# Performance work log

Measured on AMD Instinct MI355X. Metric: run time of the kernel, lower is better.

The kernel has to match this reference:

```python
import jax, jax.numpy as jnp
import numpy as np

N = 10000      # nodes
S = 4          # num_samples (walks per node)
L = 8          # walk length
F_IN = 128     # in_features == out_features (required by SelfSupervise fc)
H = 128        # out_features (GRU hidden)
ORIG = 64      # original_features
SUB = 100      # self-supervision subsample


def _gru(x, h0, Wih, Whh, bih, bhh):
    """Single-layer unidirectional GRU. x: (L, *batch, F); h0: (*batch, H)."""
    def step(hprev, xt):
        gi = xt @ Wih.T + bih            # (*batch, 3H)
        gh = hprev @ Whh.T + bhh
        ir, iz, inn = jnp.split(gi, 3, axis=-1)
        hr, hz, hn = jnp.split(gh, 3, axis=-1)
        r = jax.nn.sigmoid(ir + hr)
        z = jax.nn.sigmoid(iz + hz)
        n = jnp.tanh(inn + r * hn)
        hnew = (1.0 - z) * n + z * hprev
        return hnew, hnew
    hT, ys = jax.lax.scan(step, h0, x)
    return ys, hT                         # ys: (L, *batch, H), hT: (*batch, H)


def setup_inputs() -> dict:
    key = jax.random.key(0)
    ks = jax.random.split(key, 14)
    s = 0.1  # weight scale for numerical sanity
    return {
        "h":     jax.random.normal(ks[0], (N, F_IN), jnp.float32),
        "y0":    jax.random.uniform(ks[1], (N, ORIG), jnp.float32),  # binary-ish targets in [0,1]
        "Wih_w": s * jax.random.normal(ks[2], (3 * H, L), jnp.float32),
        "Whh_w": s * jax.random.normal(ks[3], (3 * H, H), jnp.float32),
        "bih_w": s * jax.random.normal(ks[4], (3 * H,), jnp.float32),
        "bhh_w": s * jax.random.normal(ks[5], (3 * H,), jnp.float32),
        "Wih":   s * jax.random.normal(ks[6], (3 * H, F_IN + H), jnp.float32),
        "Whh":   s * jax.random.normal(ks[7], (3 * H, H), jnp.float32),
        "bih":   s * jax.random.normal(ks[8], (3 * H,), jnp.float32),
        "bhh":   s * jax.random.normal(ks[9], (3 * H,), jnp.float32),
        "W_ss":  s * jax.random.normal(ks[10], (ORIG, F_IN), jnp.float32),
        "b_ss":  s * jax.random.normal(ks[11], (ORIG,), jnp.float32),
        "walks": jax.random.randint(ks[12], (S, N, L), 0, N),
        "idxs":  jax.random.randint(ks[13], (SUB,), 0, N),
    }


def reference(h, y0, Wih_w, Whh_w, bih_w, bhh_w, Wih, Whh, bih, bhh, W_ss, b_ss, walks, idxs):
    # uniqueness: index of first occurrence of each node within its walk, in [0, L)
    uniq = jnp.argmax(walks[..., :, None] == walks[..., None, :], axis=-1)  # (S, N, L)
    walks_f = jnp.flip(walks, axis=-1)
    uniq_f = jnp.flip(uniq, axis=-1)
    u1h = jax.nn.one_hot(uniq_f, L, dtype=h.dtype)          # (S, N, L, L)

    hw = jnp.take(h, walks_f, axis=0)                       # (S, N, L, F_IN) gather

    h0 = jnp.zeros((S, N, H), dtype=h.dtype)
    x_walk = jnp.moveaxis(u1h, -2, 0)                       # (L, S, N, L)
    y_walk, h_walk = _gru(x_walk, h0, Wih_w, Whh_w, bih_w, bhh_w)  # (L,S,N,H), (S,N,H)
    # torch: h_walk.mean(0, keepdim=True) over layer dim of size 1 -> identity

    x_main = jnp.concatenate([jnp.moveaxis(hw, -2, 0), y_walk], axis=-1)  # (L, S, N, F_IN+H)
    y_seq, hT = _gru(x_main, h_walk, Wih, Whh, bih, bhh)    # (L,S,N,H), (S,N,H)
    y = jnp.moveaxis(y_seq, 0, -2)                          # (S, N, L, H)

    # self-supervision: subsample nodes, next-step BCE
    y_t = jnp.take(y0, walks_f, axis=0)[:, idxs, 1:, :]     # (S, SUB, L-1, ORIG)
    y_hat = y[:, idxs, :-1, :] @ W_ss.T + b_ss              # (S, SUB, L-1, ORIG)
    pos_w = 1.0 / jnp.mean(y_t)
    loss = jnp.mean(pos_w * y_t * jax.nn.softplus(-y_hat)
                    + (1.0 - y_t) * jax.nn.softplus(y_hat))

    # torch: h.mean(0) over layer dim of size 1 -> hT; activation = Identity; dropout = eval
    return hT, loss
```

## Files before the change

kernel.cpp:

```cpp
#include <hip/hip_runtime.h>
#include <math.h>

#define NN    10000
#define SSS   4
#define LL    8
#define HH    128
#define NSEQ  40000
#define SUBN  100
#define ORIGF 64
#define MA    32
#define TA    512

typedef unsigned short u16;
typedef short bf16x8 __attribute__((ext_vector_type(8)));
typedef float f32x4 __attribute__((ext_vector_type(4)));

#define L2E 1.4426950408889634f

#define WL_OFF    0
#define BWRZ_OFF  6144
#define BWIN_OFF  7168
#define BWHN_OFF  7680
#define BMRZ_OFF  8192
#define BMIN_OFF  9216
#define BMHN_OFF  9728
#define HB_OFF    10240
#define HBBUF     2176
#define HB_STR    136
#define HB_SSTR   (2*HBBUF)
#define XB_OFF    27648
#define XB_STR    136
#define XB_SSTR   (128*136)
#define SCR_OFF   97280
#define SSH_STR   132
#define SWF_OFF   114176
#define SUF_OFF   115200
#define SCNT_OFF  116224
#define SANY_OFF  116352
#define LDS_TOTAL 116384

#define WB_BYTE_OFF 64
#define W_HHW_N 49152
#define W_HH_N  49152
#define W_IH_N  98304
#define W_TOTAL (W_HHW_N + W_HH_N + W_IH_N)
#define WS_NEED ((size_t)WB_BYTE_OFF + (size_t)W_TOTAL * 2 + (size_t)NN * HH * 2)

__device__ __forceinline__ float bf2f(u16 u) {
  return __uint_as_float(((unsigned)u) << 16);
}
__device__ __forceinline__ u16 f2bf(float f) {
  unsigned u = __float_as_uint(f);
  u += 0x7fffu + ((u >> 16) & 1u);
  return (u16)(u >> 16);
}
__device__ __forceinline__ bf16x8 pack8(float4 v0, float4 v1) {
  bf16x8 r;
  r[0] = (short)f2bf(v0.x); r[1] = (short)f2bf(v0.y);
  r[2] = (short)f2bf(v0.z); r[3] = (short)f2bf(v0.w);
  r[4] = (short)f2bf(v1.x); r[5] = (short)f2bf(v1.y);
  r[6] = (short)f2bf(v1.z); r[7] = (short)f2bf(v1.w);
  return r;
}
__device__ __forceinline__ float sig2_(float xs) {
  return __builtin_amdgcn_rcpf(1.f + __builtin_amdgcn_exp2f(-xs));
}
__device__ __forceinline__ float tanh2_(float xs) {
  return 1.f - 2.f * __builtin_amdgcn_rcpf(__builtin_amdgcn_exp2f(xs) + 1.f);
}
__device__ __forceinline__ float softplusf_(float x) {
  return fmaxf(x, 0.f) + log1pf(__expf(-fabsf(x)));
}

__global__ void k_zero(float* ws) {
  if (threadIdx.x < 4) ws[threadIdx.x] = 0.f;
}

__global__ void k_prep(const float* __restrict__ whhw, const float* __restrict__ whh,
                       const float* __restrict__ wih, float* __restrict__ ws) {
  const int i = blockIdx.x * 256 + threadIdx.x;
  u16* wb = (u16*)((char*)ws + WB_BYTE_OFF);
  if (i < W_HHW_N) {
    const int row = i >> 7;
    wb[i] = f2bf(whhw[i] * ((row < 256) ? L2E : 2.f * L2E));
  } else if (i < W_HHW_N + W_HH_N) {
    const int j = i - W_HHW_N, row = j >> 7;
    wb[i] = f2bf(whh[j] * ((row < 256) ? L2E : 2.f * L2E));
  } else {
    const int j = i - W_HHW_N - W_HH_N, row = j >> 8;
    wb[i] = f2bf(wih[j] * ((row < 256) ? L2E : 2.f * L2E));
  }
}

__global__ void k_prep_h(const float* __restrict__ h, float* __restrict__ ws) {
  const int i = blockIdx.x * 256 + threadIdx.x;
  u16* hb16 = (u16*)((char*)ws + WB_BYTE_OFF) + W_TOTAL;
  hb16[i] = f2bf(h[i]);
}

template<bool BF>
__global__ __launch_bounds__(TA, 2) void k_rum(
    const float* __restrict__ hfeat, const float* __restrict__ y0,
    const float* __restrict__ WihW,  const float* __restrict__ bihW,
    const float* __restrict__ bhhW,
    const float* __restrict__ bih,   const float* __restrict__ bhh,
    const float* __restrict__ W_ss,  const float* __restrict__ b_ss,
    const int* __restrict__ walks,   const int* __restrict__ idxs,
    float* __restrict__ out, float* __restrict__ ws)
{
  extern __shared__ char sm[];
  u16*   WLb  = (u16*)(sm + WL_OFF);
  float* bwrz = (float*)(sm + BWRZ_OFF);
  float* bwin = (float*)(sm + BWIN_OFF);
  float* bwhn = (float*)(sm + BWHN_OFF);
  float* bmrz = (float*)(sm + BMRZ_OFF);
  float* bmin = (float*)(sm + BMIN_OFF);
  float* bmhn = (float*)(sm + BMHN_OFF);
  u16*   hb   = (u16*)(sm + HB_OFF);
  u16*   xb   = (u16*)(sm + XB_OFF);
  float* scr  = (float*)(sm + SCR_OFF);
  int*   swf  = (int*)(sm + SWF_OFF);
  int*   suf  = (int*)(sm + SUF_OFF);
  int*   scnt = (int*)(sm + SCNT_OFF);
  int*   sany = (int*)(sm + SANY_OFF);

  const u16* wb     = (const u16*)((const char*)ws + WB_BYTE_OFF);
  const u16* whhw_b = wb;
  const u16* whh_b  = wb + W_HHW_N;
  const u16* wih_b  = wb + W_HHW_N + W_HH_N;
  const u16* hf16   = wb + W_TOTAL;

  const int tid = threadIdx.x;
  const int lane = tid & 63, c = lane & 15, qd = lane >> 4;
  const int wv = tid >> 6;
  const int i0 = wv * 16 + c;
  const int q0 = blockIdx.x * MA;

  if (tid < MA) {
    const int m = tid;
    scnt[m] = 0;
    const int q = q0 + m;
    int w[LL];
    #pragma unroll
    for (int l = 0; l < LL; ++l) w[l] = walks[q * LL + l];
    #pragma unroll
    for (int l = 0; l < LL; ++l) {
      int u = l;
      #pragma unroll
      for (int l2 = LL - 1; l2 >= 0; --l2) if (w[l2] == w[l]) u = l2;
      swf[m * LL + (LL - 1 - l)] = w[l];
      suf[m * LL + (LL - 1 - l)] = u;
    }
  }
  if (tid == 0) *sany = 0;
  for (int idx = tid; idx < 3072; idx += TA)
    WLb[idx] = f2bf(WihW[idx] * ((idx < 2048) ? L2E : 2.f * L2E));
  if (tid < 256) {
    bwrz[tid] = (bihW[tid] + bhhW[tid]) * L2E;
    bmrz[tid] = (bih[tid] + bhh[tid]) * L2E;
  }
  if (tid < 128) {
    bwin[tid] = 2.f * L2E * bihW[256 + tid]; bwhn[tid] = 2.f * L2E * bhhW[256 + tid];
    bmin[tid] = 2.f * L2E * bih[256 + tid];  bmhn[tid] = 2.f * L2E * bhh[256 + tid];
  }
  __syncthreads();

  for (int p = tid; p < MA * SUBN; p += TA) {
    const int m = p / SUBN, i = p % SUBN;
    if (idxs[i] == (q0 + m) % NN) { atomicAdd(&scnt[m], 1); *sany = 1; }
  }

  const float bw1 = bwrz[i0], bw2 = bwrz[HH + i0], bw3 = bwin[i0], bw4 = bwhn[i0];
  const float bm1 = bmrz[i0], bm2 = bmrz[HH + i0], bm3 = bmin[i0], bm4 = bmhn[i0];

  float hreg[2][4] = {{0.f, 0.f, 0.f, 0.f}, {0.f, 0.f, 0.f, 0.f}};

  {
    bf16x8 BA[3][4];
    #pragma unroll
    for (int tl = 0; tl < 3; ++tl) {
      const int row = (tl * 8 + wv) * 16 + c;
      #pragma unroll
      for (int k = 0; k < 4; ++k)
        BA[tl][k] = *(const bf16x8*)(whhw_b + row * HH + k * 32 + qd * 8);
    }
    #pragma unroll 2
    for (int t = 0; t < LL; ++t) {
      f32x4 D[2][3];
      #pragma unroll
      for (int s = 0; s < 2; ++s) {
        #pragma unroll
        for (int tl = 0; tl < 3; ++tl) D[s][tl] = (f32x4){0.f, 0.f, 0.f, 0.f};
        if (t > 0) {
          const u16* hbc = hb + s * HB_SSTR + (t & 1) * HBBUF;
          bf16x8 a[4];
          #pragma unroll
          for (int k = 0; k < 4; ++k)
            a[k] = *(const bf16x8*)(hbc + c * HB_STR + k * 32 + qd * 8);
          #pragma unroll
          for (int tl = 0; tl < 3; ++tl) {
            f32x4 d = D[s][tl];
            #pragma unroll
            for (int k = 0; k < 4; ++k)
              d = __builtin_amdgcn_mfma_f32_16x16x32_bf16(a[k], BA[tl][k], d, 0, 0, 0);
            D[s][tl] = d;
          }
        }
      }
      #pragma unroll
      for (int s = 0; s < 2; ++s) {
        u16* hbn = hb + s * HB_SSTR + ((t + 1) & 1) * HBBUF;
        u16* xbs = xb + s * XB_SSTR;
        #pragma unroll
        for (int reg = 0; reg < 4; ++reg) {
          const int ml = qd * 4 + reg;
          const int u = suf[(s * 16 + ml) * LL + t];
          const float r = sig2_(bf2f(WLb[i0 * LL + u]) + D[s][0][reg] + bw1);
          const float z = sig2_(bf2f(WLb[(HH + i0) * LL + u]) + D[s][1][reg] + bw2);
          const float n = tanh2_(bf2f(WLb[(2 * HH + i0) * LL + u]) + bw3
                                 + r * (D[s][2][reg] + bw4));
          const float hn = n + z * (hreg[s][reg] - n);
          hreg[s][reg] = hn;
          const u16 hv = f2bf(hn);
          hbn[ml * HB_STR + i0] = hv;
          xbs[(t * 16 + ml) * XB_STR + i0] = hv;
        }
      }
      __syncthreads();
    }
  }

  const bool anyf = (*sany != 0);

  bf16x8 BW[3][8], BC[3][4];
  #pragma unroll
  for (int tl = 0; tl < 3; ++tl) {
    const int row = (tl * 8 + wv) * 16 + c;
    #pragma unroll
    for (int kk = 0; kk < 8; ++kk)
      BW[tl][kk] = *(const bf16x8*)(wih_b + row * 256 + kk * 32 + qd * 8);
    #pragma unroll
    for (int k = 0; k < 4; ++k)
      BC[tl][k] = *(const bf16x8*)(whh_b + row * HH + k * 32 + qd * 8);
  }

  float pAcc = 0.f, pBcc = 0.f, pScc = 0.f;

  #pragma unroll 2
  for (int t = 0; t < LL; ++t) {
    f32x4 Drz[2][2];
    f32x4 Dnr[2];
    f32x4 Dni[2];
    #pragma unroll
    for (int s = 0; s < 2; ++s) {
      const int node = swf[(s * 16 + c) * LL + t];
      bf16x8 ah[4];
      if constexpr (BF) {
        const u16* hp = hf16 + (size_t)node * HH + qd * 8;
        #pragma unroll
        for (int k = 0; k < 4; ++k) ah[k] = *(const bf16x8*)(hp + k * 32);
      } else {
        const float* hp = hfeat + (size_t)node * HH + qd * 8;
        #pragma unroll
        for (int k = 0; k < 4; ++k)
          ah[k] = pack8(*(const float4*)(hp + k * 32),
                        *(const float4*)(hp + k * 32 + 4));
      }
      const u16* xbs = xb + s * XB_SSTR;
      bf16x8 ay[4];
      #pragma unroll
      for (int k = 0; k < 4; ++k)
        ay[k] = *(const bf16x8*)(xbs + (t * 16 + c) * XB_STR + k * 32 + qd * 8);
      const u16* hbc = hb + s * HB_SSTR + (t & 1) * HBBUF;
      bf16x8 a[4];
      #pragma unroll
      for (int k = 0; k < 4; ++k)
        a[k] = *(const bf16x8*)(hbc + c * HB_STR + k * 32 + qd * 8);
      #pragma unroll
      for (int tl = 0; tl < 2; ++tl) {
        f32x4 d = {0.f, 0.f, 0.f, 0.f};
        #pragma unroll
        for (int k = 0; k < 4; ++k)
          d = __builtin_amdgcn_mfma_f32_16x16x32_bf16(a[k], BC[tl][k], d, 0, 0, 0);
        #pragma unroll
        for (int k = 0; k < 4; ++k)
          d = __builtin_amdgcn_mfma_f32_16x16x32_bf16(ah[k], BW[tl][k], d, 0, 0, 0);
        #pragma unroll
        for (int k = 0; k < 4; ++k)
          d = __builtin_amdgcn_mfma_f32_16x16x32_bf16(ay[k], BW[tl][4 + k], d, 0, 0, 0);
        Drz[s][tl] = d;
      }
      {
        f32x4 dr = {0.f, 0.f, 0.f, 0.f}, di = {0.f, 0.f, 0.f, 0.f};
        #pragma unroll
        for (int k = 0; k < 4; ++k)
          dr = __builtin_amdgcn_mfma_f32_16x16x32_bf16(a[k], BC[2][k], dr, 0, 0, 0);
        #pragma unroll
        for (int k = 0; k < 4; ++k)
          di = __builtin_amdgcn_mfma_f32_16x16x32_bf16(ah[k], BW[2][k], di, 0, 0, 0);
        #pragma unroll
        for (int k = 0; k < 4; ++k)
          di = __builtin_amdgcn_mfma_f32_16x16x32_bf16(ay[k], BW[2][4 + k], di, 0, 0, 0);
        Dnr[s] = dr; Dni[s] = di;
      }
    }
    #pragma unroll
    for (int s = 0; s < 2; ++s) {
      u16* hbn = hb + s * HB_SSTR + ((t + 1) & 1) * HBBUF;
      #pragma unroll
      for (int reg = 0; reg < 4; ++reg) {
        const int ml = qd * 4 + reg;
        const float r = sig2_(Drz[s][0][reg] + bm1);
        const float z = sig2_(Drz[s][1][reg] + bm2);
        const float n = tanh2_(Dni[s][reg] + bm3 + r * (Dnr[s][reg] + bm4));
        const float hn = n + z * (hreg[s][reg] - n);
        hreg[s][reg] = hn;
        hbn[ml * HB_STR + i0] = f2bf(hn);
      }
    }

    if (t < LL - 1 && anyf) {
      #pragma unroll
      for (int s = 0; s < 2; ++s)
        #pragma unroll
        for (int reg = 0; reg < 4; ++reg)
          scr[(s * 16 + qd * 4 + reg) * SSH_STR + i0] = hreg[s][reg];
      __syncthreads();
      for (int idx = tid; idx < MA * ORIGF; idx += TA) {
        const int m = idx >> 6, o = idx & 63;
        const int cnt = scnt[m];
        if (cnt > 0) {
          const float* wr = W_ss + o * HH;
          float acc = b_ss[o];
          #pragma unroll 1
          for (int kc = 0; kc < HH; kc += 8) {
            const float4 wa = *(const float4*)(wr + kc);
            const float4 wb4 = *(const float4*)(wr + kc + 4);
            const float4 xa = *(const float4*)(&scr[m * SSH_STR + kc]);
            const float4 xv = *(const float4*)(&scr[m * SSH_STR + kc + 4]);
            acc = fmaf(wa.x, xa.x, acc); acc = fmaf(wa.y, xa.y, acc);
            acc = fmaf(wa.z, xa.z, acc); acc = fmaf(wa.w, xa.w, acc);
            acc = fmaf(wb4.x, xv.x, acc); acc = fmaf(wb4.y, xv.y, acc);
            acc = fmaf(wb4.z, xv.z, acc); acc = fmaf(wb4.w, xv.w, acc);
          }
          const float fc = (float)cnt;
          const float yt = y0[(size_t)swf[m * LL + t + 1] * ORIGF + o];
          pAcc += fc * yt * softplusf_(-acc);
          pBcc += fc * (1.f - yt) * softplusf_(acc);
          pScc += fc * yt;
        }
      }
    }
    __syncthreads();
  }

  #pragma unroll
  for (int s = 0; s < 2; ++s)
    #pragma unroll
    for (int reg = 0; reg < 4; ++reg)
      out[(size_t)(q0 + s * 16 + qd * 4 + reg) * HH + i0] = hreg[s][reg];

  if (anyf) {
    float* red = (float*)(sm + SCR_OFF);
    red[tid] = pAcc; red[TA + tid] = pBcc; red[2 * TA + tid] = pScc;
    __syncthreads();
    if (wv == 0) {
      float a = 0.f, b = 0.f, s = 0.f;
      for (int k2 = lane; k2 < TA; k2 += 64) {
        a += red[k2]; b += red[TA + k2]; s += red[2 * TA + k2];
      }
      #pragma unroll
      for (int off = 32; off > 0; off >>= 1) {
        a += __shfl_down(a, off); b += __shfl_down(b, off); s += __shfl_down(s, off);
      }
      if (lane == 0) {
        atomicAdd(&ws[1], a); atomicAdd(&ws[2], b); atomicAdd(&ws[3], s);
      }
    }
  }
}

__global__ void k_final(const float* __restrict__ ws, float* __restrict__ out) {
  if (threadIdx.x == 0) {
    const float cnt = (float)(SSS * SUBN * (LL - 1) * ORIGF);
    const float pos_w = cnt / ws[3];
    const float loss = (pos_w * ws[1] + ws[2]) / cnt;
    out[NSEQ * HH] = loss;
  }
}

extern "C" void kernel_launch(void* const* d_in, const int* in_sizes, int n_in,
                              void* d_out, int out_size, void* d_ws, size_t ws_size,
                              hipStream_t stream) {
  const float* hfeat = (const float*)d_in[0];
  const float* y0    = (const float*)d_in[1];
  const float* Wih_w = (const float*)d_in[2];
  const float* Whh_w = (const float*)d_in[3];
  const float* bih_w = (const float*)d_in[4];
  const float* bhh_w = (const float*)d_in[5];
  const float* Wih   = (const float*)d_in[6];
  const float* Whh   = (const float*)d_in[7];
  const float* bih   = (const float*)d_in[8];
  const float* bhh   = (const float*)d_in[9];
  const float* W_ss  = (const float*)d_in[10];
  const float* b_ss  = (const float*)d_in[11];
  const int* walks = (const int*)d_in[12];
  const int* idxs  = (const int*)d_in[13];
  float* out = (float*)d_out;
  float* ws = (float*)d_ws;

  const bool bf = (ws_size >= WS_NEED);

  (void)hipFuncSetAttribute((const void*)k_rum<true>,
                            hipFuncAttributeMaxDynamicSharedMemorySize, LDS_TOTAL);
  (void)hipFuncSetAttribute((const void*)k_rum<false>,
                            hipFuncAttributeMaxDynamicSharedMemorySize, LDS_TOTAL);

  k_zero<<<1, 64, 0, stream>>>(ws);
  k_prep<<<W_TOTAL / 256, 256, 0, stream>>>(Whh_w, Whh, Wih, ws);
  if (bf) k_prep_h<<<(NN * HH) / 256, 256, 0, stream>>>(hfeat, ws);

  const int grid = NSEQ / MA;
  if (bf)
    k_rum<true><<<grid, TA, LDS_TOTAL, stream>>>(hfeat, y0, Wih_w, bih_w, bhh_w,
                                                 bih, bhh, W_ss, b_ss,
                                                 walks, idxs, out, ws);
  else
    k_rum<false><<<grid, TA, LDS_TOTAL, stream>>>(hfeat, y0, Wih_w, bih_w, bhh_w,
                                                  bih, bhh, W_ss, b_ss,
                                                  walks, idxs, out, ws);

  k_final<<<1, 64, 0, stream>>>(ws, out);
}
```

Measured before the change: 426.9 us.

## Process 48 sequences per block and drop fp32 scratch staging for self-supervision

Raises the number of walk sequences per workgroup from 32 to 48 (three 16-row MFMA subtiles), so each block amortises its register-resident weight fragments over more rows and the grid shrinks. The per-subtile loop now interleaves MFMA and gate math instead of splitting them into two phases, which keeps accumulator register pressure lower. The fp32 scratch copy used for the self-supervision head is removed; it reads the bf16 hidden state buffer directly, which frees LDS and lowers precision of that path. Bounds checks handle the partial last block, and LDS use rises to about 144KB, which may reduce occupancy.

```diff
diff --git a/kernel.cpp b/kernel.cpp
--- a/kernel.cpp
+++ b/kernel.cpp
@@ -8,7 +8,8 @@
 #define NSEQ  40000
 #define SUBN  100
 #define ORIGF 64
-#define MA    32
+#define MA    48
+#define NS    3
 #define TA    512
 
 typedef unsigned short u16;
@@ -28,16 +29,14 @@
 #define HBBUF     2176
 #define HB_STR    136
 #define HB_SSTR   (2*HBBUF)
-#define XB_OFF    27648
+#define XB_OFF    36352
 #define XB_STR    136
 #define XB_SSTR   (128*136)
-#define SCR_OFF   97280
-#define SSH_STR   132
-#define SWF_OFF   114176
-#define SUF_OFF   115200
-#define SCNT_OFF  116224
-#define SANY_OFF  116352
-#define LDS_TOTAL 116384
+#define SWF_OFF   140800
+#define SUF_OFF   142336
+#define SCNT_OFF  143872
+#define SANY_OFF  144064
+#define LDS_TOTAL 144128
 
 #define WB_BYTE_OFF 64
 #define W_HHW_N 49152
@@ -118,7 +117,6 @@
   float* bmhn = (float*)(sm + BMHN_OFF);
   u16*   hb   = (u16*)(sm + HB_OFF);
   u16*   xb   = (u16*)(sm + XB_OFF);
-  float* scr  = (float*)(sm + SCR_OFF);
   int*   swf  = (int*)(sm + SWF_OFF);
   int*   suf  = (int*)(sm + SUF_OFF);
   int*   scnt = (int*)(sm + SCNT_OFF);
@@ -140,16 +138,21 @@
     const int m = tid;
     scnt[m] = 0;
     const int q = q0 + m;
-    int w[LL];
-    #pragma unroll
-    for (int l = 0; l < LL; ++l) w[l] = walks[q * LL + l];
-    #pragma unroll
-    for (int l = 0; l < LL; ++l) {
-      int u = l;
-      #pragma unroll
-      for (int l2 = LL - 1; l2 >= 0; --l2) if (w[l2] == w[l]) u = l2;
-      swf[m * LL + (LL - 1 - l)] = w[l];
-      suf[m * LL + (LL - 1 - l)] = u;
+    if (q < NSEQ) {
+      int w[LL];
+      #pragma unroll
+      for (int l = 0; l < LL; ++l) w[l] = walks[q * LL + l];
+      #pragma unroll
+      for (int l = 0; l < LL; ++l) {
+        int u = l;
+        #pragma unroll
+        for (int l2 = LL - 1; l2 >= 0; --l2) if (w[l2] == w[l]) u = l2;
+        swf[m * LL + (LL - 1 - l)] = w[l];
+        suf[m * LL + (LL - 1 - l)] = u;
+      }
+    } else {
+      #pragma unroll
+      for (int l = 0; l < LL; ++l) { swf[m * LL + l] = 0; suf[m * LL + l] = 0; }
     }
   }
   if (tid == 0) *sany = 0;
@@ -167,13 +170,19 @@
 
   for (int p = tid; p < MA * SUBN; p += TA) {
     const int m = p / SUBN, i = p % SUBN;
-    if (idxs[i] == (q0 + m) % NN) { atomicAdd(&scnt[m], 1); *sany = 1; }
+    if ((q0 + m) < NSEQ && idxs[i] == (q0 + m) % NN) {
+      atomicAdd(&scnt[m], 1); *sany = 1;
+    }
   }
 
   const float bw1 = bwrz[i0], bw2 = bwrz[HH + i0], bw3 = bwin[i0], bw4 = bwhn[i0];
   const float bm1 = bmrz[i0], bm2 = bmrz[HH + i0], bm3 = bmin[i0], bm4 = bmhn[i0];
 
-  float hreg[2][4] = {{0.f, 0.f, 0.f, 0.f}, {0.f, 0.f, 0.f, 0.f}};
+  float hreg[NS][4];
+  #pragma unroll
+  for (int s = 0; s < NS; ++s)
+    #pragma unroll
+    for (int r2 = 0; r2 < 4; ++r2) hreg[s][r2] = 0.f;
 
   {
     bf16x8 BA[3][4];
@@ -186,11 +195,11 @@
     }
     #pragma unroll 2
     for (int t = 0; t < LL; ++t) {
-      f32x4 D[2][3];
-      #pragma unroll
-      for (int s = 0; s < 2; ++s) {
-        #pragma unroll
-        for (int tl = 0; tl < 3; ++tl) D[s][tl] = (f32x4){0.f, 0.f, 0.f, 0.f};
+      #pragma unroll
+      for (int s = 0; s < NS; ++s) {
+        f32x4 D[3];
+        #pragma unroll
+        for (int tl = 0; tl < 3; ++tl) D[tl] = (f32x4){0.f, 0.f, 0.f, 0.f};
         if (t > 0) {
           const u16* hbc = hb + s * HB_SSTR + (t & 1) * HBBUF;
           bf16x8 a[4];
@@ -199,26 +208,23 @@
             a[k] = *(const bf16x8*)(hbc + c * HB_STR + k * 32 + qd * 8);
           #pragma unroll
           for (int tl = 0; tl < 3; ++tl) {
-            f32x4 d = D[s][tl];
+            f32x4 d = D[tl];
             #pragma unroll
             for (int k = 0; k < 4; ++k)
               d = __builtin_amdgcn_mfma_f32_16x16x32_bf16(a[k], BA[tl][k], d, 0, 0, 0);
-            D[s][tl] = d;
+            D[tl] = d;
           }
         }
-      }
-      #pragma unroll
-      for (int s = 0; s < 2; ++s) {
         u16* hbn = hb + s * HB_SSTR + ((t + 1) & 1) * HBBUF;
         u16* xbs = xb + s * XB_SSTR;
         #pragma unroll
         for (int reg = 0; reg < 4; ++reg) {
           const int ml = qd * 4 + reg;
           const int u = suf[(s * 16 + ml) * LL + t];
-          const float r = sig2_(bf2f(WLb[i0 * LL + u]) + D[s][0][reg] + bw1);
-          const float z = sig2_(bf2f(WLb[(HH + i0) * LL + u]) + D[s][1][reg] + bw2);
+          const float r = sig2_(bf2f(WLb[i0 * LL + u]) + D[0][reg] + bw1);
+          const float z = sig2_(bf2f(WLb[(HH + i0) * LL + u]) + D[1][reg] + bw2);
           const float n = tanh2_(bf2f(WLb[(2 * HH + i0) * LL + u]) + bw3
-                                 + r * (D[s][2][reg] + bw4));
+                                 + r * (D[2][reg] + bw4));
           const float hn = n + z * (hreg[s][reg] - n);
           hreg[s][reg] = hn;
           const u16 hv = f2bf(hn);
@@ -248,11 +254,8 @@
 
   #pragma unroll 2
   for (int t = 0; t < LL; ++t) {
-    f32x4 Drz[2][2];
-    f32x4 Dnr[2];
-    f32x4 Dni[2];
-    #pragma unroll
-    for (int s = 0; s < 2; ++s) {
+    #pragma unroll
+    for (int s = 0; s < NS; ++s) {
       const int node = swf[(s * 16 + c) * LL + t];
       bf16x8 ah[4];
       if constexpr (BF) {
@@ -276,6 +279,8 @@
       #pragma unroll
       for (int k = 0; k < 4; ++k)
         a[k] = *(const bf16x8*)(hbc + c * HB_STR + k * 32 + qd * 8);
+
+      f32x4 Drz[2], Dnr, Dni;
       #pragma unroll
       for (int tl = 0; tl < 2; ++tl) {
         f32x4 d = {0.f, 0.f, 0.f, 0.f};
@@ -288,7 +293,7 @@
         #pragma unroll
         for (int k = 0; k < 4; ++k)
           d = __builtin_amdgcn_mfma_f32_16x16x32_bf16(ay[k], BW[tl][4 + k], d, 0, 0, 0);
-        Drz[s][tl] = d;
+        Drz[tl] = d;
       }
       {
         f32x4 dr = {0.f, 0.f, 0.f, 0.f}, di = {0.f, 0.f, 0.f, 0.f};
@@ -301,18 +306,15 @@
         #pragma unroll
         for (int k = 0; k < 4; ++k)
           di = __builtin_amdgcn_mfma_f32_16x16x32_bf16(ay[k], BW[2][4 + k], di, 0, 0, 0);
-        Dnr[s] = dr; Dni[s] = di;
-      }
-    }
-    #pragma unroll
-    for (int s = 0; s < 2; ++s) {
+        Dnr = dr; Dni = di;
+      }
       u16* hbn = hb + s * HB_SSTR + ((t + 1) & 1) * HBBUF;
       #pragma unroll
       for (int reg = 0; reg < 4; ++reg) {
         const int ml = qd * 4 + reg;
-        const float r = sig2_(Drz[s][0][reg] + bm1);
-        const float z = sig2_(Drz[s][1][reg] + bm2);
-        const float n = tanh2_(Dni[s][reg] + bm3 + r * (Dnr[s][reg] + bm4));
+        const float r = sig2_(Drz[0][reg] + bm1);
+        const float z = sig2_(Drz[1][reg] + bm2);
+        const float n = tanh2_(Dni[reg] + bm3 + r * (Dnr[reg] + bm4));
         const float hn = n + z * (hreg[s][reg] - n);
         hreg[s][reg] = hn;
         hbn[ml * HB_STR + i0] = f2bf(hn);
@@ -320,28 +322,28 @@
     }
 
     if (t < LL - 1 && anyf) {
-      #pragma unroll
-      for (int s = 0; s < 2; ++s)
-        #pragma unroll
-        for (int reg = 0; reg < 4; ++reg)
-          scr[(s * 16 + qd * 4 + reg) * SSH_STR + i0] = hreg[s][reg];
       __syncthreads();
       for (int idx = tid; idx < MA * ORIGF; idx += TA) {
         const int m = idx >> 6, o = idx & 63;
         const int cnt = scnt[m];
         if (cnt > 0) {
+          const u16* hrow = hb + (m >> 4) * HB_SSTR + ((t + 1) & 1) * HBBUF
+                          + (m & 15) * HB_STR;
           const float* wr = W_ss + o * HH;
           float acc = b_ss[o];
           #pragma unroll 1
           for (int kc = 0; kc < HH; kc += 8) {
             const float4 wa = *(const float4*)(wr + kc);
             const float4 wb4 = *(const float4*)(wr + kc + 4);
-            const float4 xa = *(const float4*)(&scr[m * SSH_STR + kc]);
-            const float4 xv = *(const float4*)(&scr[m * SSH_STR + kc + 4]);
-            acc = fmaf(wa.x, xa.x, acc); acc = fmaf(wa.y, xa.y, acc);
-            acc = fmaf(wa.z, xa.z, acc); acc = fmaf(wa.w, xa.w, acc);
-            acc = fmaf(wb4.x, xv.x, acc); acc = fmaf(wb4.y, xv.y, acc);
-            acc = fmaf(wb4.z, xv.z, acc); acc = fmaf(wb4.w, xv.w, acc);
+            const bf16x8 xv = *(const bf16x8*)(hrow + kc);
+            acc = fmaf(wa.x, bf2f((u16)xv[0]), acc);
+            acc = fmaf(wa.y, bf2f((u16)xv[1]), acc);
+            acc = fmaf(wa.z, bf2f((u16)xv[2]), acc);
+            acc = fmaf(wa.w, bf2f((u16)xv[3]), acc);
+            acc = fmaf(wb4.x, bf2f((u16)xv[4]), acc);
+            acc = fmaf(wb4.y, bf2f((u16)xv[5]), acc);
+            acc = fmaf(wb4.z, bf2f((u16)xv[6]), acc);
+            acc = fmaf(wb4.w, bf2f((u16)xv[7]), acc);
           }
           const float fc = (float)cnt;
           const float yt = y0[(size_t)swf[m * LL + t + 1] * ORIGF + o];
@@ -355,13 +357,15 @@
   }
 
   #pragma unroll
-  for (int s = 0; s < 2; ++s)
-    #pragma unroll
-    for (int reg = 0; reg < 4; ++reg)
-      out[(size_t)(q0 + s * 16 + qd * 4 + reg) * HH + i0] = hreg[s][reg];
+  for (int s = 0; s < NS; ++s)
+    #pragma unroll
+    for (int reg = 0; reg < 4; ++reg) {
+      const int q = q0 + s * 16 + qd * 4 + reg;
+      if (q < NSEQ) out[(size_t)q * HH + i0] = hreg[s][reg];
+    }
 
   if (anyf) {
-    float* red = (float*)(sm + SCR_OFF);
+    float* red = (float*)(sm + WL_OFF);
     red[tid] = pAcc; red[TA + tid] = pBcc; red[2 * TA + tid] = pScc;
     __syncthreads();
     if (wv == 0) {
@@ -420,7 +424,7 @@
   k_prep<<<W_TOTAL / 256, 256, 0, stream>>>(Whh_w, Whh, Wih, ws);
   if (bf) k_prep_h<<<(NN * HH) / 256, 256, 0, stream>>>(hfeat, ws);
 
-  const int grid = NSEQ / MA;
+  const int grid = (NSEQ + MA - 1) / MA;
   if (bf)
     k_rum<true><<<grid, TA, LDS_TOTAL, stream>>>(hfeat, y0, Wih_w, bih_w, bhh_w,
                                                  bih, bhh, W_ss, b_ss,
```

New measurement: 391.1 us. 1.09x faster.
